# Performance work log

Measured on AMD Instinct MI355X. Metric: run time of the kernel, lower is better.

The kernel has to match this reference:

```python
import jax, jax.numpy as jnp
import numpy as np

DIM = 128

def _dwconv(x, w, b, pad):
    # x: [N,C,H,W], w: [C,1,kh,kw] depthwise (feature_group_count=C)
    y = jax.lax.conv_general_dilated(
        x, w, window_strides=(1, 1), padding=pad,
        dimension_numbers=('NCHW', 'OIHW', 'NCHW'),
        feature_group_count=x.shape[1])
    return y + b[None, :, None, None]

def setup_inputs() -> dict:
    key = jax.random.key(0)
    ks = jax.random.split(key, 13)
    d = DIM
    s = lambda k, shape, fan: jax.random.normal(k, shape, jnp.float32) * (1.0 / np.sqrt(fan))
    return {
        'x': jax.random.normal(ks[0], (16, d, 128, 128), jnp.float32),
        'w0':   s(ks[1], (d, 1, 3, 3), 9),   'b0':   jnp.zeros((d,), jnp.float32),
        'w0_1': s(ks[2], (d, 1, 1, 5), 5),   'b0_1': jnp.zeros((d,), jnp.float32),
        'w0_2': s(ks[3], (d, 1, 5, 1), 5),   'b0_2': jnp.zeros((d,), jnp.float32),
        'w1_1': s(ks[4], (d, 1, 1, 11), 11), 'b1_1': jnp.zeros((d,), jnp.float32),
        'w1_2': s(ks[5], (d, 1, 11, 1), 11), 'b1_2': jnp.zeros((d,), jnp.float32),
        'w3':   s(ks[6], (d, d, 1, 1), d),   'b3':   jnp.zeros((d,), jnp.float32),
    }

def reference(x, w0, b0, w0_1, b0_1, w0_2, b0_2, w1_1, b1_1, w1_2, b1_2, w3, b3):
    x_33  = _dwconv(x, w0, b0, ((1, 1), (1, 1)))
    x_15  = _dwconv(_dwconv(x, w0_1, b0_1, ((0, 0), (2, 2))), w0_2, b0_2, ((2, 2), (0, 0)))
    x_111 = _dwconv(_dwconv(x, w1_1, b1_1, ((0, 0), (5, 5))), w1_2, b1_2, ((5, 5), (0, 0)))
    add = x_33 + x_15 + x_111
    # 1x1 pointwise conv == channel mixing einsum
    mixer = jnp.einsum('nchw,oc->nohw', add, w3[:, :, 0, 0]) + b3[None, :, None, None]
    return mixer * x
```

## Files before the change

kernel.cpp:

```cpp
#include <hip/hip_runtime.h>
#include <stdint.h>

using f4v = __attribute__((ext_vector_type(4))) float;
using s8v = __attribute__((ext_vector_type(8))) short;

constexpr int C_ = 128, H_ = 128, W_ = 128, HW_ = H_ * W_;
constexpr int S_ = 4;
constexpr int OROWS = H_ / S_;
constexpr int CHB = 4;
constexpr int TPB = 512;
static_assert(OROWS == 32, "bias table indexing assumes 32 rows/block");

__device__ __forceinline__ unsigned f2bf(float f) {
  union { float f; unsigned u; } v; v.f = f;
  return (v.u + 0x7FFFu + ((v.u >> 16) & 1u)) >> 16;
}

__device__ __forceinline__ float sgpr(float v) {
  return __int_as_float(__builtin_amdgcn_readfirstlane(__float_as_int(v)));
}

__global__ __launch_bounds__(TPB) void k_dw(
    const float* __restrict__ x,
    const float* __restrict__ w0,  const float* __restrict__ b0,
    const float* __restrict__ w01, const float* __restrict__ b01,
    const float* __restrict__ w02, const float* __restrict__ b02,
    const float* __restrict__ w11, const float* __restrict__ b11,
    const float* __restrict__ w12, const float* __restrict__ b12,
    unsigned short* __restrict__ ws)
{
  __shared__ float xs[CHB][16][144];
  __shared__ unsigned short ebuf[16][CHB][128];
  __shared__ float bias_row[CHB][OROWS];

  const int t = threadIdx.x;
  const int yb = blockIdx.x, g = blockIdx.y, n = blockIdx.z;
  const int ch = t >> 7, xl = t & 127;
  const int c0 = g * CHB, c = c0 + ch;

  const int obase = yb * OROWS;
  const int oend  = obase + OROWS;
  const int sbase = (obase >= 5) ? (obase - 5) : 0;
  const int lastrow = (oend + 4 <= H_ - 1) ? (oend + 4) : (H_ - 1);
  const int nrows = lastrow - sbase + 1;
  const int nchunk = (nrows + 15) >> 4;

  float w0t[9], w01t[5], w02t[5], w11t[11], w12t[11];
#pragma unroll
  for (int k = 0; k < 9; ++k)  w0t[k] = sgpr(w0[c * 9 + k]);
#pragma unroll
  for (int k = 0; k < 5; ++k)  { w01t[k] = sgpr(w01[c * 5 + k]); w02t[k] = sgpr(w02[c * 5 + k]); }
#pragma unroll
  for (int k = 0; k < 11; ++k) { w11t[k] = sgpr(w11[c * 11 + k]); w12t[k] = sgpr(w12[c * 11 + k]); }

  if (t < CHB * OROWS) {
    const int cb = t >> 5, oo = t & 31;
    const int y = obase + oo, cc = c0 + cb;
    float s5 = 0.f, s11 = 0.f;
#pragma unroll
    for (int k = 0; k < 5; ++k)  if ((unsigned)(y - 2 + k) < 128u) s5  += w02[cc * 5 + k];
#pragma unroll
    for (int k = 0; k < 11; ++k) if ((unsigned)(y - 5 + k) < 128u) s11 += w12[cc * 11 + k];
    bias_row[cb][oo] = b0[cc] + b02[cc] + b12[cc] + b01[cc] * s5 + b11[cc] * s11;
  }

  if (t < 256) {
    const int zc = t >> 6, zr = (t >> 2) & 15, zq = t & 3;
    const int col = (zq < 2) ? zq * 4 : 136 + (zq - 2) * 4;
    *(float4*)&xs[zc][zr][col] = make_float4(0.f, 0.f, 0.f, 0.f);
  }

  float acc[16];
#pragma unroll
  for (int i = 0; i < 16; ++i) acc[i] = 0.f;

  unsigned short* wsp = ws + (size_t)(n * 32 + g) * HW_ * 4;

  for (int cidx = 0; cidx < nchunk; ++cidx) {
    const int r0g = sbase + cidx * 16;
    const int rem_rows = nrows - cidx * 16;
    const int rlim = rem_rows < 16 ? rem_rows : 16;
    __syncthreads();
#pragma unroll
    for (int i = 0; i < 4; ++i) {
      const int id = i * TPB + t;
      const int chs = id >> 9;
      const int rs  = (id >> 5) & 15;
      const int c4  = id & 31;
      float4 v = make_float4(0.f, 0.f, 0.f, 0.f);
      if (rs < rlim)
        v = *(const float4*)(x + (size_t)((n * C_ + c0 + chs) * H_ + r0g + rs) * W_ + c4 * 4);
      *(float4*)&xs[chs][rs][8 + c4 * 4] = v;
    }
    __syncthreads();
#pragma unroll
    for (int rr = 0; rr < 16; ++rr) {
      if (rr < rlim) {
        float win[11];
#pragma unroll
        for (int k = 0; k < 11; ++k) win[k] = xs[ch][rr][xl + 3 + k];
        float h11 = w11t[0] * win[0];
#pragma unroll
        for (int k = 1; k < 11; ++k) h11 += w11t[k] * win[k];
        float h5 = w01t[0] * win[3];
#pragma unroll
        for (int k = 1; k < 5; ++k) h5 += w01t[k] * win[3 + k];
        float r0v = w0t[0] * win[4] + w0t[1] * win[5] + w0t[2] * win[6];
        float r1v = w0t[3] * win[4] + w0t[4] * win[5] + w0t[5] * win[6];
        float r2v = w0t[6] * win[4] + w0t[7] * win[5] + w0t[8] * win[6];
#pragma unroll
        for (int tt = 0; tt < 11; ++tt) acc[(rr + 5 - tt) & 15] += w12t[tt] * h11;
#pragma unroll
        for (int tt = 0; tt < 5; ++tt)  acc[(rr + 2 - tt) & 15] += w02t[tt] * h5;
        acc[(rr + 1) & 15]  += r0v;
        acc[rr & 15]        += r1v;
        acc[(rr + 15) & 15] += r2v;
        const int o_e = r0g + rr - 5;
        const int slot = (rr + 11) & 15;
        if (o_e >= obase)
          ebuf[rr][ch][xl] = (unsigned short)f2bf(acc[slot] + bias_row[ch][o_e - obase]);
        acc[slot] = 0.f;
      }
    }
    __syncthreads();
    for (int id = t; id < 2048; id += TPB) {
      const int orr = id >> 7, px = id & 127;
      const int o = r0g + orr - 5;
      if (orr < rlim && o >= obase) {
        uint2 pk;
        pk.x = ebuf[orr][0][px] | ((unsigned)ebuf[orr][1][px] << 16);
        pk.y = ebuf[orr][2][px] | ((unsigned)ebuf[orr][3][px] << 16);
        *(uint2*)(wsp + ((size_t)o * W_ + px) * 4) = pk;
      }
    }
  }
  if (oend == H_) {
    __syncthreads();
#pragma unroll
    for (int orr = 0; orr < 5; ++orr) {
      const int o = H_ - 5 + orr;
      const int slot = (o - sbase) & 15;
      ebuf[orr][ch][xl] = (unsigned short)f2bf(acc[slot] + bias_row[ch][o - obase]);
    }
    __syncthreads();
    for (int id = t; id < 640; id += TPB) {
      const int orr = id >> 7, px = id & 127;
      const int o = H_ - 5 + orr;
      uint2 pk;
      pk.x = ebuf[orr][0][px] | ((unsigned)ebuf[orr][1][px] << 16);
      pk.y = ebuf[orr][2][px] | ((unsigned)ebuf[orr][3][px] << 16);
      *(uint2*)(wsp + ((size_t)o * W_ + px) * 4) = pk;
    }
  }
}

constexpr int PXB = 64;

__global__ __launch_bounds__(64) void k_mix(
    const float* __restrict__ x,
    const float* __restrict__ w3, const float* __restrict__ b3,
    const unsigned short* __restrict__ ws,
    float* __restrict__ out)
{
  const int t = threadIdx.x;
  const int wv = blockIdx.y;
  const int lane = t & 63, q = lane >> 4, lp = lane & 15;
  const int n = blockIdx.z;
  const int px0 = blockIdx.x * PXB;

  s8v A[2][4];
  float b3v[2][4];
#pragma unroll
  for (int m = 0; m < 2; ++m) {
    const int o = 32 * wv + 16 * m + lp;
#pragma unroll
    for (int ks = 0; ks < 4; ++ks) {
      const float* src = w3 + o * 128 + ks * 32 + q * 8;
      float4 f0 = *(const float4*)src;
      float4 f1 = *(const float4*)(src + 4);
      union { s8v v; unsigned u[4]; } pk;
      pk.u[0] = f2bf(f0.x) | (f2bf(f0.y) << 16);
      pk.u[1] = f2bf(f0.z) | (f2bf(f0.w) << 16);
      pk.u[2] = f2bf(f1.x) | (f2bf(f1.y) << 16);
      pk.u[3] = f2bf(f1.z) | (f2bf(f1.w) << 16);
      A[m][ks] = pk.v;
    }
#pragma unroll
    for (int r = 0; r < 4; ++r) b3v[m][r] = b3[32 * wv + 16 * m + 4 * q + r];
  }

  const unsigned short* wsn = ws + (size_t)n * 32 * HW_ * 4;

#pragma unroll
  for (int npg = 0; npg < PXB / 16; ++npg) {
    const int pp = px0 + npg * 16 + lp;
    s8v B[4];
#pragma unroll
    for (int ks = 0; ks < 4; ++ks) {
      const int gg8 = ks * 4 + q;
      const unsigned short* gsrc = wsn + ((size_t)(gg8 * 2) * HW_ + pp) * 4;
      union { s8v v; uint2 u2[2]; } pk;
      pk.u2[0] = *(const uint2*)gsrc;
      pk.u2[1] = *(const uint2*)(gsrc + (size_t)HW_ * 4);
      B[ks] = pk.v;
    }
    float xv[2][4];
#pragma unroll
    for (int m = 0; m < 2; ++m)
#pragma unroll
      for (int r = 0; r < 4; ++r) {
        const int o = 32 * wv + 16 * m + 4 * q + r;
        xv[m][r] = x[((size_t)(n * C_ + o) << 14) + pp];
      }
    f4v acc[2] = {{0.f,0.f,0.f,0.f},{0.f,0.f,0.f,0.f}};
#pragma unroll
    for (int ks = 0; ks < 4; ++ks) {
#pragma unroll
      for (int m = 0; m < 2; ++m)
        acc[m] = __builtin_amdgcn_mfma_f32_16x16x32_bf16(A[m][ks], B[ks], acc[m], 0, 0, 0);
    }
#pragma unroll
    for (int m = 0; m < 2; ++m)
#pragma unroll
      for (int r = 0; r < 4; ++r) {
        const int o = 32 * wv + 16 * m + 4 * q + r;
        const size_t idx = ((size_t)(n * C_ + o) << 14) + pp;
        out[idx] = (acc[m][r] + b3v[m][r]) * xv[m][r];
      }
  }
}

extern "C" void kernel_launch(void* const* d_in, const int* in_sizes, int n_in,
                              void* d_out, int out_size, void* d_ws, size_t ws_size,
                              hipStream_t stream) {
  const float* x   = (const float*)d_in[0];
  const float* w0  = (const float*)d_in[1];
  const float* b0  = (const float*)d_in[2];
  const float* w01 = (const float*)d_in[3];
  const float* b01 = (const float*)d_in[4];
  const float* w02 = (const float*)d_in[5];
  const float* b02 = (const float*)d_in[6];
  const float* w11 = (const float*)d_in[7];
  const float* b11 = (const float*)d_in[8];
  const float* w12 = (const float*)d_in[9];
  const float* b12 = (const float*)d_in[10];
  const float* w3  = (const float*)d_in[11];
  const float* b3  = (const float*)d_in[12];
  unsigned short* ws = (unsigned short*)d_ws;
  float* out = (float*)d_out;

  dim3 g1(S_, 32, 16);
  k_dw<<<g1, TPB, 0, stream>>>(x, w0, b0, w01, b01, w02, b02, w11, b11, w12, b12, ws);

  dim3 g2(HW_ / PXB, 4, 16);
  k_mix<<<g2, 64, 0, stream>>>(x, w3, b3, ws, out);
}
```

Before: 358.8 us.

## Store depthwise output as plain NCHW bf16 and gather channels in mixer

The depthwise kernel now writes each bf16 result straight to global memory in channel-planar layout. This drops the shared-memory staging buffer, its extra barriers, and the 4-channel interleaved packing. The mixer kernel now builds each MFMA B operand from eight separate 2-byte loads spread across channel planes and packs them in registers. The aim is to cut the first kernel's sync and LDS overhead. The cost is narrow 2-byte stores and 2-byte gather loads in place of 8-byte vector accesses.

```diff
diff --git a/kernel.cpp b/kernel.cpp
--- a/kernel.cpp
+++ b/kernel.cpp
@@ -30,7 +30,6 @@
     unsigned short* __restrict__ ws)
 {
   __shared__ float xs[CHB][16][144];
-  __shared__ unsigned short ebuf[16][CHB][128];
   __shared__ float bias_row[CHB][OROWS];
 
   const int t = threadIdx.x;
@@ -74,7 +73,7 @@
 #pragma unroll
   for (int i = 0; i < 16; ++i) acc[i] = 0.f;
 
-  unsigned short* wsp = ws + (size_t)(n * 32 + g) * HW_ * 4;
+  unsigned short* wsd = ws + (size_t)(n * C_ + c) * HW_ + xl;
 
   for (int cidx = 0; cidx < nchunk; ++cidx) {
     const int r0g = sbase + cidx * 16;
@@ -118,38 +117,19 @@
         const int o_e = r0g + rr - 5;
         const int slot = (rr + 11) & 15;
         if (o_e >= obase)
-          ebuf[rr][ch][xl] = (unsigned short)f2bf(acc[slot] + bias_row[ch][o_e - obase]);
+          wsd[(size_t)o_e * W_] =
+              (unsigned short)f2bf(acc[slot] + bias_row[ch][o_e - obase]);
         acc[slot] = 0.f;
       }
     }
-    __syncthreads();
-    for (int id = t; id < 2048; id += TPB) {
-      const int orr = id >> 7, px = id & 127;
-      const int o = r0g + orr - 5;
-      if (orr < rlim && o >= obase) {
-        uint2 pk;
-        pk.x = ebuf[orr][0][px] | ((unsigned)ebuf[orr][1][px] << 16);
-        pk.y = ebuf[orr][2][px] | ((unsigned)ebuf[orr][3][px] << 16);
-        *(uint2*)(wsp + ((size_t)o * W_ + px) * 4) = pk;
-      }
-    }
   }
   if (oend == H_) {
-    __syncthreads();
 #pragma unroll
     for (int orr = 0; orr < 5; ++orr) {
       const int o = H_ - 5 + orr;
       const int slot = (o - sbase) & 15;
-      ebuf[orr][ch][xl] = (unsigned short)f2bf(acc[slot] + bias_row[ch][o - obase]);
-    }
-    __syncthreads();
-    for (int id = t; id < 640; id += TPB) {
-      const int orr = id >> 7, px = id & 127;
-      const int o = H_ - 5 + orr;
-      uint2 pk;
-      pk.x = ebuf[orr][0][px] | ((unsigned)ebuf[orr][1][px] << 16);
-      pk.y = ebuf[orr][2][px] | ((unsigned)ebuf[orr][3][px] << 16);
-      *(uint2*)(wsp + ((size_t)o * W_ + px) * 4) = pk;
+      wsd[(size_t)o * W_] =
+          (unsigned short)f2bf(acc[slot] + bias_row[ch][o - obase]);
     }
   }
 }
@@ -189,7 +169,7 @@
     for (int r = 0; r < 4; ++r) b3v[m][r] = b3[32 * wv + 16 * m + 4 * q + r];
   }
 
-  const unsigned short* wsn = ws + (size_t)n * 32 * HW_ * 4;
+  const unsigned short* wsn = ws + (size_t)n * C_ * HW_;
 
 #pragma unroll
   for (int npg = 0; npg < PXB / 16; ++npg) {
@@ -197,11 +177,20 @@
     s8v B[4];
 #pragma unroll
     for (int ks = 0; ks < 4; ++ks) {
-      const int gg8 = ks * 4 + q;
-      const unsigned short* gsrc = wsn + ((size_t)(gg8 * 2) * HW_ + pp) * 4;
-      union { s8v v; uint2 u2[2]; } pk;
-      pk.u2[0] = *(const uint2*)gsrc;
-      pk.u2[1] = *(const uint2*)(gsrc + (size_t)HW_ * 4);
+      const unsigned short* base = wsn + (size_t)(ks * 32 + q * 8) * HW_ + pp;
+      unsigned v0 = base[0];
+      unsigned v1 = base[(size_t)HW_];
+      unsigned v2 = base[(size_t)HW_ * 2];
+      unsigned v3 = base[(size_t)HW_ * 3];
+      unsigned v4 = base[(size_t)HW_ * 4];
+      unsigned v5 = base[(size_t)HW_ * 5];
+      unsigned v6 = base[(size_t)HW_ * 6];
+      unsigned v7 = base[(size_t)HW_ * 7];
+      union { s8v v; unsigned u[4]; } pk;
+      pk.u[0] = v0 | (v1 << 16);
+      pk.u[1] = v2 | (v3 << 16);
+      pk.u[2] = v4 | (v5 << 16);
+      pk.u[3] = v6 | (v7 << 16);
       B[ks] = pk.v;
     }
     float xv[2][4];
```

Measured after the change: 379.9 us. +5.9%, slower.
